# Kernel optimization log

Hardware: AMD Instinct MI355X
Metric: run time of the kernel (lower is better)

Reference implementation:

```python
import jax, jax.numpy as jnp
import numpy as np
import math

SENT_DIM = 1024
HIDDEN_DIM = 1024
NUM_HEADS = 8
ALIGN_DIM = HIDDEN_DIM // NUM_HEADS  # 128
N_SENT = 4096
N_KNOW = 4096


def setup_inputs() -> dict:
    key = jax.random.key(0)
    ks = jax.random.split(key, 12)
    sentences = jax.random.normal(ks[0], (N_SENT, SENT_DIM), dtype=jnp.float32)
    knowledge = jax.random.normal(ks[1], (N_KNOW, SENT_DIM), dtype=jnp.float32)
    # binary multiplicative mask over knowledge entries, broadcast over sentence rows
    mask = (jax.random.uniform(ks[2], (N_KNOW,)) > 0.5).astype(jnp.float32)
    lim_p = 1.0 / math.sqrt(SENT_DIM)
    # per-head projections, stacked: [H, sent_dim, align_dim]
    Ws = jax.random.uniform(ks[3], (NUM_HEADS, SENT_DIM, ALIGN_DIM), minval=-lim_p, maxval=lim_p)
    bs = jax.random.uniform(ks[4], (NUM_HEADS, ALIGN_DIM), minval=-lim_p, maxval=lim_p)
    Wk = jax.random.uniform(ks[5], (NUM_HEADS, SENT_DIM, ALIGN_DIM), minval=-lim_p, maxval=lim_p)
    bk = jax.random.uniform(ks[6], (NUM_HEADS, ALIGN_DIM), minval=-lim_p, maxval=lim_p)
    # transform MLP: Linear(H*sent_dim -> sent_dim), ReLU, (dropout=identity in eval), Linear(sent_dim -> sent_dim)
    lim1 = 1.0 / math.sqrt(NUM_HEADS * SENT_DIM)
    W1 = jax.random.uniform(ks[7], (NUM_HEADS * SENT_DIM, SENT_DIM), minval=-lim1, maxval=lim1)
    b1 = jax.random.uniform(ks[8], (SENT_DIM,), minval=-lim1, maxval=lim1)
    lim2 = 1.0 / math.sqrt(SENT_DIM)
    W2 = jax.random.uniform(ks[9], (SENT_DIM, SENT_DIM), minval=-lim2, maxval=lim2)
    b2 = jax.random.uniform(ks[10], (SENT_DIM,), minval=-lim2, maxval=lim2)
    return {"sentences": sentences, "knowledge": knowledge, "mask": mask,
            "Ws": Ws, "bs": bs, "Wk": Wk, "bk": bk,
            "W1": W1, "b1": b1, "W2": W2, "b2": b2}


def reference(sentences, knowledge, mask, Ws, bs, Wk, bk, W1, b1, W2, b2):
    # Batched over heads (original loops in Python over heads)
    S = jnp.einsum('nd,hde->hne', sentences, Ws) + bs[:, None, :]   # [H, Ns, A]
    K = jnp.einsum('md,hde->hme', knowledge, Wk) + bk[:, None, :]   # [H, Nk, A]
    scores = jnp.einsum('hne,hme->hnm', S, K) / jnp.sqrt(jnp.float32(ALIGN_DIM))
    attn = jax.nn.softmax(scores, axis=-1)                          # softmax over knowledge dim
    attn = attn * mask[None, None, :]                               # post-softmax multiplicative mask
    head_out = jnp.einsum('hnm,md->hnd', attn, knowledge)           # [H, Ns, sent_dim]
    # concat heads along feature dim: [Ns, H*sent_dim]
    concat = jnp.transpose(head_out, (1, 0, 2)).reshape(head_out.shape[1], -1)
    h = jax.nn.relu(concat @ W1 + b1)                               # dropout identity in eval
    output = h @ W2 + b2                                            # [Ns, sent_dim]
    # weights cat along dim 0: [H*Ns, Nk]
    weights = attn.reshape(-1, attn.shape[-1])
    return output, weights
```

## Files before the change

### kernel.cpp

```cpp
#include <hip/hip_runtime.h>
#include <hip/hip_bf16.h>

typedef __attribute__((ext_vector_type(4))) float  floatx4;
typedef __attribute__((ext_vector_type(8))) short  shortx8;
typedef __attribute__((ext_vector_type(4))) short  shortx4;

__device__ __forceinline__ short f2bf(float x) {
    union { float f; unsigned u; } v; v.f = x;
    unsigned r = v.u + 0x7FFFu + ((v.u >> 16) & 1u);
    return (short)(r >> 16);
}
__device__ __forceinline__ float bf2f(short x) {
    union { unsigned u; float f; } c; c.u = ((unsigned)(unsigned short)x) << 16;
    return c.f;
}


__global__ void cast_bf16(const float* __restrict__ src, short* __restrict__ dst, int n4) {
    int i = blockIdx.x * blockDim.x + threadIdx.x;
    if (i < n4) {
        floatx4 v = ((const floatx4*)src)[i];
        shortx4 s;
        s[0] = f2bf(v[0]); s[1] = f2bf(v[1]); s[2] = f2bf(v[2]); s[3] = f2bf(v[3]);
        ((shortx4*)dst)[i] = s;
    }
}

__global__ void transpose_cast(const float* __restrict__ src, short* __restrict__ dst,
                               int R, int C, long szSrc, long szDst) {
    __shared__ float tile[32][33];
    const float* s = src + (long)blockIdx.z * szSrc;
    short* d = dst + (long)blockIdx.z * szDst;
    int c0 = blockIdx.x * 32, r0 = blockIdx.y * 32;
    for (int i = threadIdx.y; i < 32; i += 8)
        tile[i][threadIdx.x] = s[(long)(r0 + i) * C + c0 + threadIdx.x];
    __syncthreads();
    for (int i = threadIdx.y; i < 32; i += 8)
        d[(long)(c0 + i) * R + r0 + threadIdx.x] = f2bf(tile[threadIdx.x][i]);
}


#define BM 128
#define BN 128
#define BK 32
#define LSTR 40

template<bool AF32, bool RELU, bool CF32>
__global__ __launch_bounds__(256) void gemm_nt(
    const void* __restrict__ Ap, const short* __restrict__ Bp, void* __restrict__ Cp,
    const float* __restrict__ bias, float alpha,
    int K, int lda, int ldb, int ldc,
    long sAz, long sBz, long sCz, long aHX, long sbias)
{
    __shared__ __align__(16) short As[BM * LSTR];
    __shared__ __align__(16) short Bs[BN * LSTR];

    const int t    = threadIdx.x;
    const int m0   = blockIdx.y * BM;
    const int n0   = blockIdx.x * BN;
    const int z    = blockIdx.z;
    const int wave = t >> 6, lane = t & 63;
    const int wm   = (wave & 1) * 64, wn = (wave >> 1) * 64;
    const int quad = lane >> 4, l16 = lane & 15;

    const short* Bz = Bp + (long)z * sBz;

    floatx4 acc[4][4] = {};

    for (int k0 = 0; k0 < K; k0 += BK) {
        const long hoff = (long)(k0 >> 12) * aHX;
        __syncthreads();
        if (AF32) {
            const float* Az = (const float*)Ap + (long)z * sAz + hoff;
            #pragma unroll
            for (int p = 0; p < 4; ++p) {
                int idx = (p * 256 + t) * 4;
                int row = idx >> 5, kk = idx & 31;
                floatx4 v = *(const floatx4*)(Az + (long)(m0 + row) * lda + (k0 + kk));
                shortx4 sv;
                sv[0] = f2bf(v[0]); sv[1] = f2bf(v[1]); sv[2] = f2bf(v[2]); sv[3] = f2bf(v[3]);
                *(shortx4*)(&As[row * LSTR + kk]) = sv;
            }
        } else {
            const short* Az = (const short*)Ap + (long)z * sAz + hoff;
            #pragma unroll
            for (int p = 0; p < 2; ++p) {
                int idx = (p * 256 + t) * 8;
                int row = idx >> 5, kk = idx & 31;
                *(shortx8*)(&As[row * LSTR + kk]) =
                    *(const shortx8*)(Az + (long)(m0 + row) * lda + (k0 + kk));
            }
        }
        #pragma unroll
        for (int p = 0; p < 2; ++p) {
            int idx = (p * 256 + t) * 8;
            int row = idx >> 5, kk = idx & 31;
            *(shortx8*)(&Bs[row * LSTR + kk]) =
                *(const shortx8*)(Bz + (long)(n0 + row) * ldb + (k0 + kk));
        }
        __syncthreads();

        shortx8 af[4], bfr[4];
        #pragma unroll
        for (int i = 0; i < 4; ++i)
            af[i] = *(const shortx8*)(&As[(wm + i * 16 + l16) * LSTR + quad * 8]);
        #pragma unroll
        for (int j = 0; j < 4; ++j)
            bfr[j] = *(const shortx8*)(&Bs[(wn + j * 16 + l16) * LSTR + quad * 8]);
        #pragma unroll
        for (int i = 0; i < 4; ++i)
            #pragma unroll
            for (int j = 0; j < 4; ++j)
                acc[i][j] = __builtin_amdgcn_mfma_f32_16x16x32_bf16(af[i], bfr[j], acc[i][j], 0, 0, 0);
    }

    float bv[4];
    #pragma unroll
    for (int j = 0; j < 4; ++j)
        bv[j] = bias ? (bias + (long)z * sbias)[n0 + wn + j * 16 + l16] : 0.0f;

    #pragma unroll
    for (int i = 0; i < 4; ++i) {
        #pragma unroll
        for (int e = 0; e < 4; ++e) {
            long row = m0 + wm + i * 16 + quad * 4 + e;
            #pragma unroll
            for (int j = 0; j < 4; ++j) {
                float val = acc[i][j][e] * alpha + bv[j];
                if (RELU) val = fmaxf(val, 0.0f);
                long col = n0 + wn + j * 16 + l16;
                if (CF32) ((float*)Cp + (long)z * sCz)[row * ldc + col] = val;
                else      ((short*)Cp + (long)z * sCz)[row * ldc + col] = f2bf(val);
            }
        }
    }
}


__global__ __launch_bounds__(256) void softmax_mask(float* __restrict__ attn,
                                                    const float* __restrict__ mask) {
    float* p = attn + (long)blockIdx.x * 4096;
    const int t = threadIdx.x;
    float v[16];
    float mx = -3.4e38f;
    #pragma unroll
    for (int i = 0; i < 16; ++i) { v[i] = p[t + 256 * i]; mx = fmaxf(mx, v[i]); }
    #pragma unroll
    for (int o = 32; o > 0; o >>= 1) mx = fmaxf(mx, __shfl_down(mx, o));
    __shared__ float r1[4], r2[4];
    const int lane = t & 63, w = t >> 6;
    if (lane == 0) r1[w] = mx;
    __syncthreads();
    mx = fmaxf(fmaxf(r1[0], r1[1]), fmaxf(r1[2], r1[3]));
    float s = 0.f;
    #pragma unroll
    for (int i = 0; i < 16; ++i) { v[i] = __expf(v[i] - mx); s += v[i]; }
    #pragma unroll
    for (int o = 32; o > 0; o >>= 1) s += __shfl_down(s, o);
    if (lane == 0) r2[w] = s;
    __syncthreads();
    s = r2[0] + r2[1] + r2[2] + r2[3];
    const float inv = 1.0f / s;
    #pragma unroll
    for (int i = 0; i < 16; ++i) p[t + 256 * i] = v[i] * inv * mask[t + 256 * i];
}


__global__ __launch_bounds__(256) void reduce_heads(const short* __restrict__ part,
                                                    const float* __restrict__ b1,
                                                    short* __restrict__ h_bf) {
    int i = blockIdx.x * blockDim.x + threadIdx.x;
    float s[8] = {0,0,0,0,0,0,0,0};
    #pragma unroll
    for (int z = 0; z < 4; ++z) {
        shortx8 v = ((const shortx8*)(part + (long)z * 4194304))[i];
        #pragma unroll
        for (int e = 0; e < 8; ++e) s[e] += bf2f(v[e]);
    }
    int j0 = (i * 8) & 1023;
    shortx8 o;
    #pragma unroll
    for (int e = 0; e < 8; ++e) o[e] = f2bf(fmaxf(s[e] + b1[j0 + e], 0.f));
    ((shortx8*)h_bf)[i] = o;
}


extern "C" void kernel_launch(void* const* d_in, const int* in_sizes, int n_in,
                              void* d_out, int out_size, void* d_ws, size_t ws_size,
                              hipStream_t stream) {
    const float* sentences = (const float*)d_in[0];
    const float* knowledge = (const float*)d_in[1];
    const float* mask      = (const float*)d_in[2];
    const float* Ws        = (const float*)d_in[3];
    const float* bs        = (const float*)d_in[4];
    const float* Wk        = (const float*)d_in[5];
    const float* bk        = (const float*)d_in[6];
    const float* W1        = (const float*)d_in[7];
    const float* b1        = (const float*)d_in[8];
    const float* W2        = (const float*)d_in[9];
    const float* b2        = (const float*)d_in[10];

    float* out  = (float*)d_out;
    float* attn = out + 4194304;

    char* ws = (char*)d_ws;
    short* V_T     = (short*)(ws);
    short* W2T     = (short*)(ws + 67108864);
    short* h_bf    = (short*)(ws + 69206016);
    float* bias2   = (float*)(ws + 77594624);
    short* sent_bf = (short*)(ws + 77611008);
    short* know_bf = (short*)(ws + 85999616);
    short* WsT     = (short*)(ws + 94388224);
    short* WkT     = (short*)(ws + 96485376);
    short* W1T     = (short*)(ws + 98582528);
    short* S_bf    = (short*)(ws + 115359744);
    short* K_bf    = (short*)(ws + 123748352);
    short* part    = (short*)(ws + 77611008);

    cast_bf16<<<4096, 256, 0, stream>>>(sentences, sent_bf, 1048576);
    cast_bf16<<<4096, 256, 0, stream>>>(knowledge, know_bf, 1048576);
    transpose_cast<<<dim3(4, 32, 8),  dim3(32, 8), 0, stream>>>(Ws, WsT, 1024, 128, 131072, 131072);
    transpose_cast<<<dim3(4, 32, 8),  dim3(32, 8), 0, stream>>>(Wk, WkT, 1024, 128, 131072, 131072);
    transpose_cast<<<dim3(32, 32, 8), dim3(32, 8), 0, stream>>>(W1, W1T, 1024, 1024, 1048576, 1048576);
    transpose_cast<<<dim3(32, 32, 1), dim3(32, 8), 0, stream>>>(W2, W2T, 1024, 1024, 0, 0);
    hipMemcpyAsync(bias2,        bs, 4096, hipMemcpyDeviceToDevice, stream);
    hipMemcpyAsync(bias2 + 1024, bk, 4096, hipMemcpyDeviceToDevice, stream);

    gemm_nt<false, false, false><<<dim3(8, 32, 2), 256, 0, stream>>>(
        sent_bf, WsT, S_bf, bias2, 1.0f, 1024, 1024, 1024, 1024,
        4194304, 1048576, 4194304, 0, 1024);
    gemm_nt<false, false, false><<<dim3(32, 8, 8), 256, 0, stream>>>(
        W1T, know_bf, V_T, nullptr, 1.0f, 1024, 1024, 1024, 32768,
        1048576, 0, 4096, 0, 0);
    gemm_nt<false, false, true><<<dim3(32, 32, 8), 256, 0, stream>>>(
        S_bf, K_bf, attn, nullptr, 0.08838834764831845f, 128, 1024, 1024, 4096,
        128, 128, 16777216, 0, 0);
    softmax_mask<<<32768, 256, 0, stream>>>(attn, mask);
    gemm_nt<true, false, false><<<dim3(8, 32, 4), 256, 0, stream>>>(
        attn, V_T, part, nullptr, 1.0f, 8192, 4096, 32768, 1024,
        33554432, 8192, 4194304, 16777216 - 4096, 0);
    reduce_heads<<<2048, 256, 0, stream>>>(part, b1, h_bf);
    gemm_nt<false, false, true><<<dim3(8, 32, 1), 256, 0, stream>>>(
        h_bf, W2T, out, b2, 1.0f, 1024, 1024, 1024, 1024, 0, 0, 0, 0, 0);
}
```

Measured before the change: 1.703 ms.

## Load GEMM tiles directly to LDS with XOR swizzle and block remap

Replaces register-staged global-to-shared copies in the GEMM with global_load_lds direct-to-LDS loads, and drops the padded layout in favour of an XOR-swizzled one to avoid bank conflicts. For the fp32 attention-times-V GEMM, the fp32 tile is now kept in LDS and converted to bf16 when fragments are read, using the hardware conversion. A block-index swizzle is added for that GEMM to improve L2 reuse of the attention rows. The fp32 path doubles that GEMM's A-tile LDS footprint and repeats the conversion in each wave that reads the tile.

```diff
diff --git a/kernel.cpp b/kernel.cpp
--- a/kernel.cpp
+++ b/kernel.cpp
@@ -13,6 +13,17 @@
 __device__ __forceinline__ float bf2f(short x) {
     union { unsigned u; float f; } c; c.u = ((unsigned)(unsigned short)x) << 16;
     return c.f;
+}
+__device__ __forceinline__ short f2bf_hw(float x) {
+    union { __hip_bfloat16 h; short s; } u;
+    u.h = __float2bfloat16(x);
+    return u.s;
+}
+
+__device__ __forceinline__ void gload16(const void* g, void* l) {
+    __builtin_amdgcn_global_load_lds(
+        (const __attribute__((address_space(1))) void*)g,
+        (__attribute__((address_space(3))) void*)l, 16, 0, 0);
 }
 
 
@@ -43,70 +54,96 @@
 #define BM 128
 #define BN 128
 #define BK 32
-#define LSTR 40
-
-template<bool AF32, bool RELU, bool CF32>
+
+template<bool AF32, bool RELU, bool CF32, bool XSWZ>
 __global__ __launch_bounds__(256) void gemm_nt(
     const void* __restrict__ Ap, const short* __restrict__ Bp, void* __restrict__ Cp,
     const float* __restrict__ bias, float alpha,
     int K, int lda, int ldb, int ldc,
     long sAz, long sBz, long sCz, long aHX, long sbias)
 {
-    __shared__ __align__(16) short As[BM * LSTR];
-    __shared__ __align__(16) short Bs[BN * LSTR];
+    __shared__ __align__(16) char  AsB[AF32 ? BM * BK * 4 : BM * BK * 2];
+    __shared__ __align__(16) short Bs[BN * BK];
+    short* AsS = reinterpret_cast<short*>(AsB);
+    float* AsF = reinterpret_cast<float*>(AsB);
+
+    int bx, by, bz;
+    if constexpr (XSWZ) {
+        int id = blockIdx.x + (blockIdx.y << 3) + (blockIdx.z << 8);
+        bx = (id >> 3) & 7;
+        int g = (id & 7) | ((id >> 6) << 3);
+        by = g & 31; bz = g >> 5;
+    } else { bx = blockIdx.x; by = blockIdx.y; bz = blockIdx.z; }
 
     const int t    = threadIdx.x;
-    const int m0   = blockIdx.y * BM;
-    const int n0   = blockIdx.x * BN;
-    const int z    = blockIdx.z;
+    const int m0   = by * BM;
+    const int n0   = bx * BN;
+    const int z    = bz;
     const int wave = t >> 6, lane = t & 63;
     const int wm   = (wave & 1) * 64, wn = (wave >> 1) * 64;
     const int quad = lane >> 4, l16 = lane & 15;
+    const int wofs = t & ~63;
 
     const short* Bz = Bp + (long)z * sBz;
 
+    const int srow = t >> 2;
+    const int ssw  = ((t & 3) ^ ((t >> 3) & 3)) * 8;
+    const short* bSrc = Bz + (long)(n0 + srow) * ldb + ssw;
+
+    const short* aSrc  = nullptr;
+    const float* aSrcF = nullptr;
+    if constexpr (AF32) {
+        const float* Az = (const float*)Ap + (long)z * sAz;
+        aSrcF = Az + (long)(m0 + (t >> 3)) * lda + (((t & 7) ^ ((t >> 3) & 7)) * 4);
+    } else {
+        const short* Az = (const short*)Ap + (long)z * sAz;
+        aSrc = Az + (long)(m0 + srow) * lda + ssw;
+    }
+
+    const int ra = wm + l16, rb = wn + l16;
+    const int sa = (quad ^ ((ra >> 1) & 3)) * 8;
+    const int sb = (quad ^ ((rb >> 1) & 3)) * 8;
+    const int s0 = (((quad << 1)    ) ^ (ra & 7)) * 4;
+    const int s1 = (((quad << 1) | 1) ^ (ra & 7)) * 4;
+
     floatx4 acc[4][4] = {};
 
     for (int k0 = 0; k0 < K; k0 += BK) {
-        const long hoff = (long)(k0 >> 12) * aHX;
+        const long off = (long)k0 + (long)(k0 >> 12) * aHX;
         __syncthreads();
-        if (AF32) {
-            const float* Az = (const float*)Ap + (long)z * sAz + hoff;
+        if constexpr (AF32) {
             #pragma unroll
-            for (int p = 0; p < 4; ++p) {
-                int idx = (p * 256 + t) * 4;
-                int row = idx >> 5, kk = idx & 31;
-                floatx4 v = *(const floatx4*)(Az + (long)(m0 + row) * lda + (k0 + kk));
-                shortx4 sv;
-                sv[0] = f2bf(v[0]); sv[1] = f2bf(v[1]); sv[2] = f2bf(v[2]); sv[3] = f2bf(v[3]);
-                *(shortx4*)(&As[row * LSTR + kk]) = sv;
-            }
+            for (int p = 0; p < 4; ++p)
+                gload16(aSrcF + (long)p * 32 * lda + off,
+                        AsF + (p * 256 + wofs) * 4);
         } else {
-            const short* Az = (const short*)Ap + (long)z * sAz + hoff;
-            #pragma unroll
-            for (int p = 0; p < 2; ++p) {
-                int idx = (p * 256 + t) * 8;
-                int row = idx >> 5, kk = idx & 31;
-                *(shortx8*)(&As[row * LSTR + kk]) =
-                    *(const shortx8*)(Az + (long)(m0 + row) * lda + (k0 + kk));
+            gload16(aSrc + off,                  AsS + wofs * 8);
+            gload16(aSrc + (long)64 * lda + off, AsS + (256 + wofs) * 8);
+        }
+        gload16(bSrc + k0,                  &Bs[wofs * 8]);
+        gload16(bSrc + (long)64 * ldb + k0, &Bs[(256 + wofs) * 8]);
+        __syncthreads();
+
+        shortx8 af[4], bfr[4];
+        #pragma unroll
+        for (int i = 0; i < 4; ++i) {
+            if constexpr (AF32) {
+                const float* pf = AsF + (ra + 16 * i) * 32;
+                floatx4 f0 = *(const floatx4*)(pf + s0);
+                floatx4 f1 = *(const floatx4*)(pf + s1);
+                shortx8 s;
+                s[0] = f2bf_hw(f0[0]); s[1] = f2bf_hw(f0[1]);
+                s[2] = f2bf_hw(f0[2]); s[3] = f2bf_hw(f0[3]);
+                s[4] = f2bf_hw(f1[0]); s[5] = f2bf_hw(f1[1]);
+                s[6] = f2bf_hw(f1[2]); s[7] = f2bf_hw(f1[3]);
+                af[i] = s;
+            } else {
+                af[i] = *(const shortx8*)(AsS + (ra + 16 * i) * 32 + sa);
             }
         }
         #pragma unroll
-        for (int p = 0; p < 2; ++p) {
-            int idx = (p * 256 + t) * 8;
-            int row = idx >> 5, kk = idx & 31;
-            *(shortx8*)(&Bs[row * LSTR + kk]) =
-                *(const shortx8*)(Bz + (long)(n0 + row) * ldb + (k0 + kk));
-        }
-        __syncthreads();
-
-        shortx8 af[4], bfr[4];
-        #pragma unroll
-        for (int i = 0; i < 4; ++i)
-            af[i] = *(const shortx8*)(&As[(wm + i * 16 + l16) * LSTR + quad * 8]);
-        #pragma unroll
         for (int j = 0; j < 4; ++j)
-            bfr[j] = *(const shortx8*)(&Bs[(wn + j * 16 + l16) * LSTR + quad * 8]);
+            bfr[j] = *(const shortx8*)(&Bs[(rb + 16 * j) * 32 + sb]);
         #pragma unroll
         for (int i = 0; i < 4; ++i)
             #pragma unroll
@@ -216,6 +253,7 @@
     short* S_bf    = (short*)(ws + 115359744);
     short* K_bf    = (short*)(ws + 123748352);
     short* part    = (short*)(ws + 77611008);
+    (void)K_bf;
 
     cast_bf16<<<4096, 256, 0, stream>>>(sentences, sent_bf, 1048576);
     cast_bf16<<<4096, 256, 0, stream>>>(knowledge, know_bf, 1048576);
@@ -226,20 +264,20 @@
     hipMemcpyAsync(bias2,        bs, 4096, hipMemcpyDeviceToDevice, stream);
     hipMemcpyAsync(bias2 + 1024, bk, 4096, hipMemcpyDeviceToDevice, stream);
 
-    gemm_nt<false, false, false><<<dim3(8, 32, 2), 256, 0, stream>>>(
+    gemm_nt<false, false, false, false><<<dim3(8, 32, 2), 256, 0, stream>>>(
         sent_bf, WsT, S_bf, bias2, 1.0f, 1024, 1024, 1024, 1024,
         4194304, 1048576, 4194304, 0, 1024);
-    gemm_nt<false, false, false><<<dim3(32, 8, 8), 256, 0, stream>>>(
+    gemm_nt<false, false, false, false><<<dim3(32, 8, 8), 256, 0, stream>>>(
         W1T, know_bf, V_T, nullptr, 1.0f, 1024, 1024, 1024, 32768,
         1048576, 0, 4096, 0, 0);
-    gemm_nt<false, false, true><<<dim3(32, 32, 8), 256, 0, stream>>>(
+    gemm_nt<false, false, true, false><<<dim3(32, 32, 8), 256, 0, stream>>>(
         S_bf, K_bf, attn, nullptr, 0.08838834764831845f, 128, 1024, 1024, 4096,
         128, 128, 16777216, 0, 0);
     softmax_mask<<<32768, 256, 0, stream>>>(attn, mask);
-    gemm_nt<true, false, false><<<dim3(8, 32, 4), 256, 0, stream>>>(
+    gemm_nt<true, false, false, true><<<dim3(8, 32, 4), 256, 0, stream>>>(
         attn, V_T, part, nullptr, 1.0f, 8192, 4096, 32768, 1024,
         33554432, 8192, 4194304, 16777216 - 4096, 0);
     reduce_heads<<<2048, 256, 0, stream>>>(part, b1, h_bf);
-    gemm_nt<false, false, true><<<dim3(8, 32, 1), 256, 0, stream>>>(
+    gemm_nt<false, false, true, false><<<dim3(8, 32, 1), 256, 0, stream>>>(
         h_bf, W2T, out, b2, 1.0f, 1024, 1024, 1024, 1024, 0, 0, 0, 0, 0);
 }
```

Measured after the change: 1.605 ms. -5.7%, faster.
